# Optimization experiments

Measured on AMD Instinct MI355X. Metric: run time of the kernel, lower is better.

Reference implementation:

```python
import jax, jax.numpy as jnp
import numpy as np

NUM_HEADS = 12
HIDDEN = 768
HEAD_DIM = HIDDEN // NUM_HEADS
SCALE = HEAD_DIM ** -0.5


def setup_inputs() -> dict:
    key = jax.random.key(0)
    k1, k2, k3 = jax.random.split(key, 3)
    b, n = 2, 2048
    x = jax.random.normal(k1, (b, n, HIDDEN), dtype=jnp.float32)
    w_qkv = jax.random.normal(k2, (3 * HIDDEN, HIDDEN), dtype=jnp.float32) * (HIDDEN ** -0.5)
    w_out = jax.random.normal(k3, (HIDDEN, HIDDEN), dtype=jnp.float32) * (HIDDEN ** -0.5)
    b_out = jnp.zeros((HIDDEN,), dtype=jnp.float32)
    return {"x": x, "w_qkv": w_qkv, "w_out": w_out, "b_out": b_out}


def reference(x, w_qkv, w_out, b_out):
    b, n, h = x.shape  # [b, seq, hidden]
    # qkv linear (no bias), then 'b n (qkv heads d) -> qkv b heads n d'
    qkv = (x @ w_qkv.T).reshape(b, n, 3, NUM_HEADS, HEAD_DIM)
    qkv = qkv.transpose(2, 0, 3, 1, 4)
    q, k, v = qkv[0], qkv[1], qkv[2]  # each [b, heads, n, d]
    att = jax.nn.softmax(jnp.einsum('bhxd,bhyd->bhxy', q, k) * SCALE, axis=-1)
    out = jnp.einsum('bhxy,bhyd->bhxd', att, v)
    out = out.transpose(0, 2, 1, 3).reshape(b, n, h)  # 'b h n d -> b n (h d)'
    return out @ w_out.T + b_out
```

## Files before the change

### kernel.cpp

```cpp
#include <hip/hip_runtime.h>
#include <hip/hip_bf16.h>
#include <cstdint>
#include <cstddef>

#define SEQ    2048
#define BATCH  2
#define HID    768
#define NH     12
#define HD     64
#define QKV_N  2304

typedef __attribute__((ext_vector_type(8))) short bf16x8;
typedef __attribute__((ext_vector_type(4))) float f32x4;
typedef __attribute__((ext_vector_type(16))) float f32x16;

static __device__ __forceinline__ short f2bf(float x) {
  __hip_bfloat16 h = __float2bfloat16(x);
  short s;
  __builtin_memcpy(&s, &h, 2);
  return s;
}
static __device__ __forceinline__ float bf2f(short s) {
  __hip_bfloat16 h;
  __builtin_memcpy(&h, &s, 2);
  return __bfloat162float(h);
}

__global__ __launch_bounds__(256)
void cvt3_f32_bf16(const float* __restrict__ s0, short* __restrict__ d0,
                   const float* __restrict__ s1, short* __restrict__ d1,
                   const float* __restrict__ s2, short* __restrict__ d2) {
  int bid = blockIdx.x;
  const float* src;
  short* dst;
  if (bid < 1536)      { src = s0; dst = d0; }
  else if (bid < 2400) { src = s1; dst = d1; bid -= 1536; }
  else                 { src = s2; dst = d2; bid -= 2400; }
  const int i = (bid * 256 + threadIdx.x) * 8;
  const float4 a = *reinterpret_cast<const float4*>(src + i);
  const float4 b = *reinterpret_cast<const float4*>(src + i + 4);
  bf16x8 o;
  o[0] = f2bf(a.x); o[1] = f2bf(a.y); o[2] = f2bf(a.z); o[3] = f2bf(a.w);
  o[4] = f2bf(b.x); o[5] = f2bf(b.y); o[6] = f2bf(b.z); o[7] = f2bf(b.w);
  *reinterpret_cast<bf16x8*>(dst + i) = o;
}

template <bool BF16_OUT>
__global__ __launch_bounds__(256)
void gemm_nt_mfma(const short* __restrict__ A, const short* __restrict__ B,
                  const float* __restrict__ bias,
                  float* __restrict__ Cf, short* __restrict__ Cb,
                  int M, int N, int K) {
  __shared__ short As[128][64];
  __shared__ short Bs[128][64];

  const int t = threadIdx.x;
  const int w = t >> 6;
  const int l = t & 63;
  const int g = l >> 4;
  const int n = l & 15;

  const int m0 = blockIdx.y * 128;
  const int n0 = blockIdx.x * 128;
  const int wr = (w >> 1) * 64;
  const int wc = (w & 1) * 64;

  const int srow = w * 32 + (l >> 3);
  const int scol = (l & 7) * 8;
  const short* Ag = A + (size_t)(m0 + srow) * K + scol;
  const short* Bg = B + (size_t)(n0 + srow) * K + scol;

  f32x4 acc[4][4] = {};

  for (int k0 = 0; k0 < K; k0 += 64) {
    __syncthreads();
#pragma unroll
    for (int it = 0; it < 4; ++it) {
      __builtin_amdgcn_global_load_lds(
          (const __attribute__((address_space(1))) void*)(Ag + (size_t)(it * 8) * K + k0),
          (__attribute__((address_space(3))) void*)(&As[w * 32 + it * 8][0]),
          16, 0, 0);
    }
#pragma unroll
    for (int it = 0; it < 4; ++it) {
      __builtin_amdgcn_global_load_lds(
          (const __attribute__((address_space(1))) void*)(Bg + (size_t)(it * 8) * K + k0),
          (__attribute__((address_space(3))) void*)(&Bs[w * 32 + it * 8][0]),
          16, 0, 0);
    }
    __syncthreads();

#pragma unroll
    for (int kk = 0; kk < 2; ++kk) {
      bf16x8 af[4], bfr[4];
#pragma unroll
      for (int m = 0; m < 4; ++m)
        af[m] = *reinterpret_cast<const bf16x8*>(&As[wr + m * 16 + n][kk * 32 + g * 8]);
#pragma unroll
      for (int j = 0; j < 4; ++j)
        bfr[j] = *reinterpret_cast<const bf16x8*>(&Bs[wc + j * 16 + n][kk * 32 + g * 8]);
#pragma unroll
      for (int m = 0; m < 4; ++m)
#pragma unroll
        for (int j = 0; j < 4; ++j)
          acc[m][j] = __builtin_amdgcn_mfma_f32_16x16x32_bf16(af[m], bfr[j], acc[m][j], 0, 0, 0);
    }
  }

#pragma unroll
  for (int m = 0; m < 4; ++m) {
#pragma unroll
    for (int r = 0; r < 4; ++r) {
      const size_t row = m0 + wr + m * 16 + g * 4 + r;
#pragma unroll
      for (int j = 0; j < 4; ++j) {
        const int col = n0 + wc + j * 16 + n;
        float v = acc[m][j][r];
        if (bias) v += bias[col];
        if (BF16_OUT) Cb[row * N + col] = f2bf(v);
        else          Cf[row * N + col] = v;
      }
    }
  }
}

__global__ __launch_bounds__(256)
void gemm_nt_mfma64(const short* __restrict__ A, const short* __restrict__ B,
                    const float* __restrict__ bias, float* __restrict__ Cf,
                    int M, int N, int K) {
  __shared__ short As[64][64];
  __shared__ short Bs[64][64];

  const int t = threadIdx.x;
  const int w = t >> 6;
  const int l = t & 63;
  const int g = l >> 4;
  const int n = l & 15;

  const int m0 = blockIdx.y * 64;
  const int n0 = blockIdx.x * 64;
  const int wr = (w >> 1) * 32;
  const int wc = (w & 1) * 32;

  const int srow = t >> 3;
  const int scol = (t & 7) * 8;
  const short* Ag = A + (size_t)(m0 + srow) * K + scol;
  const short* Bg = B + (size_t)(n0 + srow) * K + scol;

  f32x4 acc[2][2] = {};

  for (int k0 = 0; k0 < K; k0 += 64) {
    __syncthreads();
#pragma unroll
    for (int it = 0; it < 2; ++it) {
      __builtin_amdgcn_global_load_lds(
          (const __attribute__((address_space(1))) void*)(Ag + (size_t)(it * 32) * K + k0),
          (__attribute__((address_space(3))) void*)(&As[w * 8 + it * 32][0]),
          16, 0, 0);
    }
#pragma unroll
    for (int it = 0; it < 2; ++it) {
      __builtin_amdgcn_global_load_lds(
          (const __attribute__((address_space(1))) void*)(Bg + (size_t)(it * 32) * K + k0),
          (__attribute__((address_space(3))) void*)(&Bs[w * 8 + it * 32][0]),
          16, 0, 0);
    }
    __syncthreads();

#pragma unroll
    for (int kk = 0; kk < 2; ++kk) {
      bf16x8 af[2], bfr[2];
#pragma unroll
      for (int m = 0; m < 2; ++m)
        af[m] = *reinterpret_cast<const bf16x8*>(&As[wr + m * 16 + n][kk * 32 + g * 8]);
#pragma unroll
      for (int j = 0; j < 2; ++j)
        bfr[j] = *reinterpret_cast<const bf16x8*>(&Bs[wc + j * 16 + n][kk * 32 + g * 8]);
#pragma unroll
      for (int m = 0; m < 2; ++m)
#pragma unroll
        for (int j = 0; j < 2; ++j)
          acc[m][j] = __builtin_amdgcn_mfma_f32_16x16x32_bf16(af[m], bfr[j], acc[m][j], 0, 0, 0);
    }
  }

#pragma unroll
  for (int m = 0; m < 2; ++m) {
#pragma unroll
    for (int r = 0; r < 4; ++r) {
      const size_t row = m0 + wr + m * 16 + g * 4 + r;
#pragma unroll
      for (int j = 0; j < 2; ++j) {
        const int col = n0 + wc + j * 16 + n;
        Cf[row * N + col] = acc[m][j][r] + bias[col];
      }
    }
  }
}

__global__ __launch_bounds__(512)
void attn_mfma(const short* __restrict__ qkv, short* __restrict__ att) {
  const int bh = blockIdx.x;
  const int qt = blockIdx.y;
  const int b  = bh / NH;
  const int h0 = bh % NH;
  const int q0 = qt * 64;

  const int t   = threadIdx.x;
  const int w   = t >> 6;
  const int l   = t & 63;
  const int hi  = l >> 5;
  const int q31 = l & 31;
  const int qq  = w >> 2;
  const int kh  = w & 3;

  __shared__ __align__(16) char smem[54272];
  short* KxL = (short*)smem;
  short* VtL = (short*)(smem + 16384);
  short* PsL = (short*)(smem + 33792);

  const short* baseq = qkv + (size_t)b * SEQ * QKV_N + h0 * HD;
  const short* Kg    = baseq + HID;
  const short* Vg    = baseq + 2 * HID;

  bf16x8 qf[4];
  {
    const short* qrow = baseq + (size_t)(q0 + qq * 32 + q31) * QKV_N;
#pragma unroll
    for (int c16 = 0; c16 < 4; ++c16) {
      bf16x8 raw = *reinterpret_cast<const bf16x8*>(qrow + c16 * 16 + hi * 8);
#pragma unroll
      for (int j = 0; j < 8; ++j) qf[c16][j] = f2bf(bf2f(raw[j]) * 0.125f);
    }
  }

  f32x16 o0 = {};
  f32x16 o1 = {};
  float mrow = -3e38f;
  float lrow = 0.f;

  const int sr   = t >> 2;
  const int sb   = t & 3;
  const int vcol = sr ^ (sb << 4);

  const int kv0  = t >> 3;
  const int dg0  = (t & 7) ^ (kv0 & 7);
  const int kv1  = kv0 + 64;
  const int dg1  = (t & 7) ^ (kv1 & 7);

  __builtin_amdgcn_global_load_lds(
      (const __attribute__((address_space(1))) void*)(Kg + (size_t)kv0 * QKV_N + dg0 * 8),
      (__attribute__((address_space(3))) void*)(KxL + w * 512), 16, 0, 0);
  __builtin_amdgcn_global_load_lds(
      (const __attribute__((address_space(1))) void*)(Kg + (size_t)kv1 * QKV_N + dg1 * 8),
      (__attribute__((address_space(3))) void*)(KxL + w * 512 + 4096), 16, 0, 0);
  bf16x8 vA, vB;
  {
    const short* vp = Vg + (size_t)sr * QKV_N + sb * 16;
    vA = *reinterpret_cast<const bf16x8*>(vp);
    vB = *reinterpret_cast<const bf16x8*>(vp + 8);
  }
  __syncthreads();

  const int krow = kh * 32 + q31;
  const int kxor = l & 7;

  for (int j = 0; j < SEQ / 128; ++j) {
    const bool have_next = (j + 1) < SEQ / 128;

#pragma unroll
    for (int idx = 0; idx < 8; ++idx) VtL[(sb * 16 + idx) * 136 + vcol]     = vA[idx];
#pragma unroll
    for (int idx = 0; idx < 8; ++idx) VtL[(sb * 16 + 8 + idx) * 136 + vcol] = vB[idx];

    f32x16 sc = {};
#pragma unroll
    for (int c16 = 0; c16 < 4; ++c16) {
      bf16x8 kb = *reinterpret_cast<const bf16x8*>(
          (const char*)KxL + krow * 128 + (((c16 * 2 + hi) ^ kxor) << 4));
      sc = __builtin_amdgcn_mfma_f32_32x32x16_bf16(kb, qf[c16], sc, 0, 0, 0);
    }
    __syncthreads();

    if (have_next) {
      const size_t rb = (size_t)(j + 1) * 128;
      __builtin_amdgcn_global_load_lds(
          (const __attribute__((address_space(1))) void*)(Kg + (rb + kv0) * QKV_N + dg0 * 8),
          (__attribute__((address_space(3))) void*)(KxL + w * 512), 16, 0, 0);
      __builtin_amdgcn_global_load_lds(
          (const __attribute__((address_space(1))) void*)(Kg + (rb + kv1) * QKV_N + dg1 * 8),
          (__attribute__((address_space(3))) void*)(KxL + w * 512 + 4096), 16, 0, 0);
      const short* vp = Vg + (rb + sr) * QKV_N + sb * 16;
      vA = *reinterpret_cast<const bf16x8*>(vp);
      vB = *reinterpret_cast<const bf16x8*>(vp + 8);
    }

    {
      float pm = fmaxf(fmaxf(sc[0], sc[1]), fmaxf(sc[2], sc[3]));
#pragma unroll
      for (int r = 4; r < 16; r += 4)
        pm = fmaxf(pm, fmaxf(fmaxf(sc[r], sc[r + 1]), fmaxf(sc[r + 2], sc[r + 3])));
      pm = fmaxf(pm, __shfl_xor(pm, 32));
      if (__any(pm - mrow > 8.f)) {
        const float mnew = fmaxf(mrow, pm);
        const float corr = __expf(mrow - mnew);
        mrow = mnew;
        lrow *= corr;
#pragma unroll
        for (int r = 0; r < 16; ++r) { o0[r] *= corr; o1[r] *= corr; }
      }
      float psum = 0.f;
#pragma unroll
      for (int rr = 0; rr < 4; ++rr) {
        const float p0 = __expf(sc[rr * 4 + 0] - mrow);
        const float p1 = __expf(sc[rr * 4 + 1] - mrow);
        const float p2 = __expf(sc[rr * 4 + 2] - mrow);
        const float p3 = __expf(sc[rr * 4 + 3] - mrow);
        psum += (p0 + p1) + (p2 + p3);
        short4 pk;
        pk.x = f2bf(p0); pk.y = f2bf(p1); pk.z = f2bf(p2); pk.w = f2bf(p3);
        *reinterpret_cast<short4*>(
            &PsL[w * 1280 + q31 * 40 + rr * 8 + hi * 4]) = pk;
      }
      lrow += psum;
    }

#pragma unroll
    for (int c = 0; c < 2; ++c) {
      bf16x8 pb = *reinterpret_cast<const bf16x8*>(
          &PsL[w * 1280 + q31 * 40 + c * 16 + hi * 8]);
      {
        const int vrow = q31;
        bf16x8 va = *reinterpret_cast<const bf16x8*>(
            &VtL[vrow * 136 + ((kh * 32 + c * 16 + hi * 8) ^ ((vrow >> 4) << 4))]);
        o0 = __builtin_amdgcn_mfma_f32_32x32x16_bf16(va, pb, o0, 0, 0, 0);
      }
      {
        const int vrow = 32 + q31;
        bf16x8 va = *reinterpret_cast<const bf16x8*>(
            &VtL[vrow * 136 + ((kh * 32 + c * 16 + hi * 8) ^ ((vrow >> 4) << 4))]);
        o1 = __builtin_amdgcn_mfma_f32_32x32x16_bf16(va, pb, o1, 0, 0, 0);
      }
    }
    __syncthreads();
  }

  lrow += __shfl_xor(lrow, 32);

  float* mbf = (float*)smem;
  const int base = (qq * 2 + (kh >> 1)) * 2176 + l * 34;
  if (kh & 1) {
#pragma unroll
    for (int r = 0; r < 16; ++r) { mbf[base + r] = o0[r]; mbf[base + 16 + r] = o1[r]; }
    mbf[base + 32] = mrow;
    mbf[base + 33] = lrow;
  }
  __syncthreads();
  if (!(kh & 1)) {
    const float m2 = mbf[base + 32];
    const float l2 = mbf[base + 33];
    const float mn = fmaxf(mrow, m2);
    const float ca = __expf(mrow - mn);
    const float cb = __expf(m2 - mn);
#pragma unroll
    for (int r = 0; r < 16; ++r) {
      o0[r] = o0[r] * ca + mbf[base + r] * cb;
      o1[r] = o1[r] * ca + mbf[base + 16 + r] * cb;
    }
    lrow = lrow * ca + l2 * cb;
    mrow = mn;
  }
  __syncthreads();
  const int base2 = qq * 2176 + l * 34;
  if (kh == 2) {
#pragma unroll
    for (int r = 0; r < 16; ++r) { mbf[base2 + r] = o0[r]; mbf[base2 + 16 + r] = o1[r]; }
    mbf[base2 + 32] = mrow;
    mbf[base2 + 33] = lrow;
  }
  __syncthreads();
  if (kh == 0) {
    const float m2 = mbf[base2 + 32];
    const float l2 = mbf[base2 + 33];
    const float mn = fmaxf(mrow, m2);
    const float ca = __expf(mrow - mn);
    const float cb = __expf(m2 - mn);
    const float lm = lrow * ca + l2 * cb;
    const float linv = 1.f / lm;
    short* orow = att + (size_t)(b * SEQ + q0 + qq * 32 + q31) * HID + h0 * HD;
#pragma unroll
    for (int rr = 0; rr < 4; ++rr) {
      short4 ov;
      ov.x = f2bf((o0[rr * 4 + 0] * ca + mbf[base2 + rr * 4 + 0] * cb) * linv);
      ov.y = f2bf((o0[rr * 4 + 1] * ca + mbf[base2 + rr * 4 + 1] * cb) * linv);
      ov.z = f2bf((o0[rr * 4 + 2] * ca + mbf[base2 + rr * 4 + 2] * cb) * linv);
      ov.w = f2bf((o0[rr * 4 + 3] * ca + mbf[base2 + rr * 4 + 3] * cb) * linv);
      *reinterpret_cast<short4*>(&orow[rr * 8 + hi * 4]) = ov;
      short4 ow;
      ow.x = f2bf((o1[rr * 4 + 0] * ca + mbf[base2 + 16 + rr * 4 + 0] * cb) * linv);
      ow.y = f2bf((o1[rr * 4 + 1] * ca + mbf[base2 + 16 + rr * 4 + 1] * cb) * linv);
      ow.z = f2bf((o1[rr * 4 + 2] * ca + mbf[base2 + 16 + rr * 4 + 2] * cb) * linv);
      ow.w = f2bf((o1[rr * 4 + 3] * ca + mbf[base2 + 16 + rr * 4 + 3] * cb) * linv);
      *reinterpret_cast<short4*>(&orow[32 + rr * 8 + hi * 4]) = ow;
    }
  }
}

extern "C" void kernel_launch(void* const* d_in, const int* in_sizes, int n_in,
                              void* d_out, int out_size, void* d_ws, size_t ws_size,
                              hipStream_t stream) {
  const float* x     = (const float*)d_in[0];
  const float* w_qkv = (const float*)d_in[1];
  const float* w_out = (const float*)d_in[2];
  const float* b_out = (const float*)d_in[3];
  float* out = (float*)d_out;

  const int NX  = BATCH * SEQ * HID;
  const int NWQ = QKV_N * HID;
  const int NWO = HID * HID;

  char* ws = (char*)d_ws;
  short* xb   = (short*)ws;  ws += (size_t)NX  * 2;
  short* wqb  = (short*)ws;  ws += (size_t)NWQ * 2;
  short* wob  = (short*)ws;  ws += (size_t)NWO * 2;
  short* qkvb = (short*)ws;  ws += (size_t)BATCH * SEQ * QKV_N * 2;
  short* attb = (short*)ws;

  cvt3_f32_bf16<<<dim3(2688), dim3(256), 0, stream>>>(x, xb, w_qkv, wqb, w_out, wob);

  gemm_nt_mfma<true><<<dim3(QKV_N / 128, (BATCH * SEQ) / 128), dim3(256), 0, stream>>>(
      xb, wqb, nullptr, nullptr, qkvb, BATCH * SEQ, QKV_N, HID);

  attn_mfma<<<dim3(BATCH * NH, SEQ / 64), dim3(512), 0, stream>>>(qkvb, attb);

  gemm_nt_mfma64<<<dim3(HID / 64, (BATCH * SEQ) / 64), dim3(256), 0, stream>>>(
      attb, wob, b_out, out, BATCH * SEQ, HID, HID);
}
```

Measured before the change: 114.9 us.

## Pre-transpose V into global memory and read V fragments directly in attention

Adds a separate kernel that writes V transposed per batch-head into workspace. The attention kernel then loads V operand fragments straight from global memory into registers instead of staging and transposing V through LDS each tile. This drops the scalar LDS transpose writes and their barrier pressure, and cuts LDS use so more blocks fit per CU (launch bounds now ask for 6). The cost is an extra kernel launch, a full extra write and read of V, and uncoalesced-ish per-iteration global loads in the inner loop that may not be hidden.

```diff
diff --git a/kernel.cpp b/kernel.cpp
--- a/kernel.cpp
+++ b/kernel.cpp
@@ -198,8 +198,43 @@
   }
 }
 
-__global__ __launch_bounds__(512)
-void attn_mfma(const short* __restrict__ qkv, short* __restrict__ att) {
+__global__ __launch_bounds__(256)
+void transpose_v(const short* __restrict__ qkv, short* __restrict__ vtg) {
+  const int bh  = blockIdx.x;
+  const int kvt = blockIdx.y;
+  const int b   = bh / NH;
+  const int h   = bh % NH;
+
+  __shared__ short Lt[64][72];
+
+  const int t  = threadIdx.x;
+  const int ry = t >> 2;
+  const int rd = (t & 3) * 16;
+
+  const short* src = qkv + (size_t)(b * SEQ + kvt * 64 + ry) * QKV_N
+                         + 2 * HID + h * HD + rd;
+  bf16x8 a0 = *reinterpret_cast<const bf16x8*>(src);
+  bf16x8 a1 = *reinterpret_cast<const bf16x8*>(src + 8);
+  *reinterpret_cast<bf16x8*>(&Lt[ry][rd])     = a0;
+  *reinterpret_cast<bf16x8*>(&Lt[ry][rd + 8]) = a1;
+  __syncthreads();
+
+  const int wd = t >> 2;
+  const int wy = (t & 3) * 16;
+  bf16x8 o0, o1;
+#pragma unroll
+  for (int j = 0; j < 8; ++j) {
+    o0[j] = Lt[wy + j][wd];
+    o1[j] = Lt[wy + 8 + j][wd];
+  }
+  short* dst = vtg + ((size_t)bh * 64 + wd) * SEQ + kvt * 64 + wy;
+  *reinterpret_cast<bf16x8*>(dst)     = o0;
+  *reinterpret_cast<bf16x8*>(dst + 8) = o1;
+}
+
+__global__ __launch_bounds__(512, 6)
+void attn_mfma(const short* __restrict__ qkv, const short* __restrict__ vtg,
+               short* __restrict__ att) {
   const int bh = blockIdx.x;
   const int qt = blockIdx.y;
   const int b  = bh / NH;
@@ -214,14 +249,13 @@
   const int qq  = w >> 2;
   const int kh  = w & 3;
 
-  __shared__ __align__(16) char smem[54272];
+  __shared__ __align__(16) char smem[36864];
   short* KxL = (short*)smem;
-  short* VtL = (short*)(smem + 16384);
-  short* PsL = (short*)(smem + 33792);
+  short* PsL = (short*)(smem + 16384);
 
   const short* baseq = qkv + (size_t)b * SEQ * QKV_N + h0 * HD;
   const short* Kg    = baseq + HID;
-  const short* Vg    = baseq + 2 * HID;
+  const short* vt_bh = vtg + (size_t)bh * 64 * SEQ;
 
   bf16x8 qf[4];
   {
@@ -239,9 +273,8 @@
   float mrow = -3e38f;
   float lrow = 0.f;
 
-  const int sr   = t >> 2;
-  const int sb   = t & 3;
-  const int vcol = sr ^ (sb << 4);
+  const short* vrow0 = vt_bh + (size_t)q31 * SEQ + kh * 32 + hi * 8;
+  const short* vrow1 = vt_bh + (size_t)(32 + q31) * SEQ + kh * 32 + hi * 8;
 
   const int kv0  = t >> 3;
   const int dg0  = (t & 7) ^ (kv0 & 7);
@@ -254,24 +287,13 @@
   __builtin_amdgcn_global_load_lds(
       (const __attribute__((address_space(1))) void*)(Kg + (size_t)kv1 * QKV_N + dg1 * 8),
       (__attribute__((address_space(3))) void*)(KxL + w * 512 + 4096), 16, 0, 0);
-  bf16x8 vA, vB;
-  {
-    const short* vp = Vg + (size_t)sr * QKV_N + sb * 16;
-    vA = *reinterpret_cast<const bf16x8*>(vp);
-    vB = *reinterpret_cast<const bf16x8*>(vp + 8);
-  }
   __syncthreads();
 
   const int krow = kh * 32 + q31;
   const int kxor = l & 7;
 
-  for (int j = 0; j < SEQ / 128; ++j) {
-    const bool have_next = (j + 1) < SEQ / 128;
-
-#pragma unroll
-    for (int idx = 0; idx < 8; ++idx) VtL[(sb * 16 + idx) * 136 + vcol]     = vA[idx];
-#pragma unroll
-    for (int idx = 0; idx < 8; ++idx) VtL[(sb * 16 + 8 + idx) * 136 + vcol] = vB[idx];
+  for (int ti = 0; ti < SEQ / 128; ++ti) {
+    const bool have_next = (ti + 1) < SEQ / 128;
 
     f32x16 sc = {};
 #pragma unroll
@@ -283,17 +305,21 @@
     __syncthreads();
 
     if (have_next) {
-      const size_t rb = (size_t)(j + 1) * 128;
+      const size_t rb = (size_t)(ti + 1) * 128;
       __builtin_amdgcn_global_load_lds(
           (const __attribute__((address_space(1))) void*)(Kg + (rb + kv0) * QKV_N + dg0 * 8),
           (__attribute__((address_space(3))) void*)(KxL + w * 512), 16, 0, 0);
       __builtin_amdgcn_global_load_lds(
           (const __attribute__((address_space(1))) void*)(Kg + (rb + kv1) * QKV_N + dg1 * 8),
           (__attribute__((address_space(3))) void*)(KxL + w * 512 + 4096), 16, 0, 0);
-      const short* vp = Vg + (rb + sr) * QKV_N + sb * 16;
-      vA = *reinterpret_cast<const bf16x8*>(vp);
-      vB = *reinterpret_cast<const bf16x8*>(vp + 8);
-    }
+    }
+
+    const short* v0p = vrow0 + ti * 128;
+    const short* v1p = vrow1 + ti * 128;
+    bf16x8 v00 = *reinterpret_cast<const bf16x8*>(v0p);
+    bf16x8 v01 = *reinterpret_cast<const bf16x8*>(v0p + 16);
+    bf16x8 v10 = *reinterpret_cast<const bf16x8*>(v1p);
+    bf16x8 v11 = *reinterpret_cast<const bf16x8*>(v1p + 16);
 
     {
       float pm = fmaxf(fmaxf(sc[0], sc[1]), fmaxf(sc[2], sc[3]));
@@ -325,22 +351,13 @@
       lrow += psum;
     }
 
-#pragma unroll
-    for (int c = 0; c < 2; ++c) {
-      bf16x8 pb = *reinterpret_cast<const bf16x8*>(
-          &PsL[w * 1280 + q31 * 40 + c * 16 + hi * 8]);
-      {
-        const int vrow = q31;
-        bf16x8 va = *reinterpret_cast<const bf16x8*>(
-            &VtL[vrow * 136 + ((kh * 32 + c * 16 + hi * 8) ^ ((vrow >> 4) << 4))]);
-        o0 = __builtin_amdgcn_mfma_f32_32x32x16_bf16(va, pb, o0, 0, 0, 0);
-      }
-      {
-        const int vrow = 32 + q31;
-        bf16x8 va = *reinterpret_cast<const bf16x8*>(
-            &VtL[vrow * 136 + ((kh * 32 + c * 16 + hi * 8) ^ ((vrow >> 4) << 4))]);
-        o1 = __builtin_amdgcn_mfma_f32_32x32x16_bf16(va, pb, o1, 0, 0, 0);
-      }
+    {
+      bf16x8 pb0 = *reinterpret_cast<const bf16x8*>(&PsL[w * 1280 + q31 * 40 + hi * 8]);
+      bf16x8 pb1 = *reinterpret_cast<const bf16x8*>(&PsL[w * 1280 + q31 * 40 + 16 + hi * 8]);
+      o0 = __builtin_amdgcn_mfma_f32_32x32x16_bf16(v00, pb0, o0, 0, 0, 0);
+      o1 = __builtin_amdgcn_mfma_f32_32x32x16_bf16(v10, pb0, o1, 0, 0, 0);
+      o0 = __builtin_amdgcn_mfma_f32_32x32x16_bf16(v01, pb1, o0, 0, 0, 0);
+      o1 = __builtin_amdgcn_mfma_f32_32x32x16_bf16(v11, pb1, o1, 0, 0, 0);
     }
     __syncthreads();
   }
@@ -424,14 +441,17 @@
   short* wqb  = (short*)ws;  ws += (size_t)NWQ * 2;
   short* wob  = (short*)ws;  ws += (size_t)NWO * 2;
   short* qkvb = (short*)ws;  ws += (size_t)BATCH * SEQ * QKV_N * 2;
-  short* attb = (short*)ws;
+  short* attb = (short*)ws;  ws += (size_t)BATCH * SEQ * HID * 2;
+  short* vtg  = (short*)ws;
 
   cvt3_f32_bf16<<<dim3(2688), dim3(256), 0, stream>>>(x, xb, w_qkv, wqb, w_out, wob);
 
   gemm_nt_mfma<true><<<dim3(QKV_N / 128, (BATCH * SEQ) / 128), dim3(256), 0, stream>>>(
       xb, wqb, nullptr, nullptr, qkvb, BATCH * SEQ, QKV_N, HID);
 
-  attn_mfma<<<dim3(BATCH * NH, SEQ / 64), dim3(512), 0, stream>>>(qkvb, attb);
+  transpose_v<<<dim3(BATCH * NH, SEQ / 64), dim3(256), 0, stream>>>(qkvb, vtg);
+
+  attn_mfma<<<dim3(BATCH * NH, SEQ / 64), dim3(512), 0, stream>>>(qkvb, vtg, attb);
 
   gemm_nt_mfma64<<<dim3(HID / 64, (BATCH * SEQ) / 64), dim3(256), 0, stream>>>(
       attb, wob, b_out, out, BATCH * SEQ, HID, HID);
```

After: 183.6 us. 59.8% more time.
